# Kernel optimization log

Hardware: AMD Instinct MI355X
Metric: run time of the kernel (lower is better)

Reference implementation:

```python
import jax, jax.numpy as jnp
import numpy as np
from jax import lax

WIN = (9, 9, 9)
EPS = 1e-05


def _sum1d(x, axis, win):
    """Sliding-window sum of size `win` along `axis`, zero-padded (SAME)."""
    pad = win // 2
    pads = [(pad, pad) if a == axis else (0, 0) for a in range(x.ndim)]
    xp = jnp.pad(x, pads)
    c = jnp.cumsum(xp, axis=axis)
    c = jnp.pad(c, [(1, 0) if a == axis else (0, 0) for a in range(x.ndim)])
    n = x.shape[axis]
    return (lax.slice_in_dim(c, win, win + n, axis=axis)
            - lax.slice_in_dim(c, 0, n, axis=axis))


def _box_sum(x):
    """Separable 3D box-filter sum == conv3d with ones([9,9,9]), SAME pad."""
    for axis, w in zip((2, 3, 4), WIN):
        x = _sum1d(x, axis, w)
    return x


def setup_inputs() -> dict:
    key = jax.random.key(0)
    k1, k2 = jax.random.split(key)
    shape = (2, 1, 128, 128, 128)
    y_pred = jax.random.normal(k1, shape, dtype=jnp.float32)
    y_true = jax.random.normal(k2, shape, dtype=jnp.float32)
    return {"y_pred": y_pred, "y_true": y_true}


def reference(y_pred, y_true):
    I = y_true.astype(jnp.float32)
    J = y_pred.astype(jnp.float32)
    win_size = float(np.prod(WIN))  # 729

    I_sum = _box_sum(I)
    J_sum = _box_sum(J)
    I2_sum = _box_sum(I * I)
    J2_sum = _box_sum(J * J)
    IJ_sum = _box_sum(I * J)

    u_I = I_sum / win_size
    u_J = J_sum / win_size

    cross = IJ_sum - u_J * I_sum - u_I * J_sum + u_I * u_J * win_size
    I_var = I2_sum - 2 * u_I * I_sum + u_I * u_I * win_size
    J_var = J2_sum - 2 * u_J * J_sum + u_J * u_J * win_size

    cc_map = cross * cross / (I_var * J_var + EPS)
    return jnp.mean(-cc_map)
```

## Files before the change

kernel.cpp:

```cpp
#include <hip/hip_runtime.h>

#define DSZ 128
#define TX 16
#define TY 16
#define PY 24
#define NVOX 4194304.0f

__global__ void ncc_zero(float* out) { out[0] = 0.0f; }

__global__ __launch_bounds__(256) void ncc_main(const float* __restrict__ Iin,
                                                const float* __restrict__ Jin,
                                                float* __restrict__ out)
{
    const int tx0 = blockIdx.x * TX;
    const int ty0 = blockIdx.y * TY;
    const int b   = blockIdx.z >> 3;
    const int tz0 = (blockIdx.z & 7) * 16;
    const int tid = threadIdx.x;
    const int lx  = tid & 15;
    const int ly  = tid >> 4;

    const float* __restrict__ Ib = Iin + b * (DSZ * DSZ * DSZ);
    const float* __restrict__ Jb = Jin + b * (DSZ * DSZ * DSZ);

    __shared__ float4 s4m[4][PY][17];
    __shared__ float4 s1v[4][PY][5];

    float rb0[9], rb1[9], rb2[9], rb3[9], rb4[9];
#pragma unroll
    for (int i = 0; i < 9; ++i) { rb0[i]=0.f; rb1[i]=0.f; rb2[i]=0.f; rb3[i]=0.f; rb4[i]=0.f; }
    float zs0=0.f, zs1=0.f, zs2=0.f, zs3=0.f, zs4=0.f;
    float acc = 0.f;

    for (int rnd = 0; rnd < 12; ++rnd) {
        if (tid < 192) {
            const int p   = (tid >= 96);
            const int t2  = tid - p * 96;
            const int r   = t2 >> 2;
            const int xg  = t2 & 3;
            const int zp  = tz0 + 2 * rnd + p - 4;
            const int gy  = ty0 + r - 4;
            const int gxb = tx0 + 4 * xg - 4;
            const bool rowok = ((unsigned)zp < (unsigned)DSZ) &&
                               ((unsigned)gy < (unsigned)DSZ);
            const int zoff = (zp * DSZ + gy) * DSZ;

            float vi[12], vj[12];
#pragma unroll
            for (int g = 0; g < 3; ++g) {
                const int gx = gxb + 4 * g;
                float4 va = make_float4(0.f, 0.f, 0.f, 0.f);
                float4 vb = va;
                if (rowok && (unsigned)gx < (unsigned)DSZ) {
                    va = *(const float4*)(Ib + zoff + gx);
                    vb = *(const float4*)(Jb + zoff + gx);
                }
                vi[4*g+0]=va.x; vi[4*g+1]=va.y; vi[4*g+2]=va.z; vi[4*g+3]=va.w;
                vj[4*g+0]=vb.x; vj[4*g+1]=vb.y; vj[4*g+2]=vb.z; vj[4*g+3]=vb.w;
            }

            float wI=0.f, wJ=0.f, wII=0.f, wJJ=0.f, wIJ=0.f;
#pragma unroll
            for (int k = 3; k < 9; ++k) {
                wI += vi[k]; wJ += vj[k];
                wII = fmaf(vi[k], vi[k], wII);
                wJJ = fmaf(vj[k], vj[k], wJJ);
                wIJ = fmaf(vi[k], vj[k], wIJ);
            }
#pragma unroll
            for (int k = 0; k < 3; ++k) {
                wI += vi[k]; wJ += vj[k];
                wII = fmaf(vi[k], vi[k], wII);
                wJJ = fmaf(vj[k], vj[k], wJJ);
                wIJ = fmaf(vi[k], vj[k], wIJ);
            }
            const int sl = (rnd & 1) * 2 + p;
            float mIJ[4];
            s4m[sl][r][4*xg] = make_float4(wI, wJ, wII, wJJ);
            mIJ[0] = wIJ;
#pragma unroll
            for (int j = 1; j < 4; ++j) {
                const float ai = vi[8+j], aj = vj[8+j];
                const float di = vi[j-1], dj = vj[j-1];
                wI += ai - di; wJ += aj - dj;
                wII += fmaf(ai, ai, -di * di);
                wJJ += fmaf(aj, aj, -dj * dj);
                wIJ += fmaf(ai, aj, -di * dj);
                s4m[sl][r][4*xg + j] = make_float4(wI, wJ, wII, wJJ);
                mIJ[j] = wIJ;
            }
            s1v[sl][r][xg] = make_float4(mIJ[0], mIJ[1], mIJ[2], mIJ[3]);
        }
        __syncthreads();

#pragma unroll
        for (int p = 0; p < 2; ++p) {
            const int sl = (rnd & 1) * 2 + p;
            float y0=0.f, y1=0.f, y2=0.f, y3=0.f, y4=0.f;
#pragma unroll
            for (int dy = 0; dy < 9; ++dy) {
                const float4 t = s4m[sl][ly + dy][lx];
                y0 += t.x; y1 += t.y; y2 += t.z; y3 += t.w;
                y4 += ((const float*)&s1v[sl][ly + dy][0])[lx];
            }

            zs0 += y0 - rb0[0]; zs1 += y1 - rb1[0]; zs2 += y2 - rb2[0];
            zs3 += y3 - rb3[0]; zs4 += y4 - rb4[0];
#pragma unroll
            for (int i = 0; i < 8; ++i) {
                rb0[i]=rb0[i+1]; rb1[i]=rb1[i+1]; rb2[i]=rb2[i+1];
                rb3[i]=rb3[i+1]; rb4[i]=rb4[i+1];
            }
            rb0[8]=y0; rb1[8]=y1; rb2[8]=y2; rb3[8]=y3; rb4[8]=y4;

            const int zi = 2 * rnd + p;
            if (zi >= 8) {
                const float inv = 1.0f / 729.0f;
                const float uI = zs0 * inv;
                const float uJ = zs1 * inv;
                const float cross = zs4 - uJ * zs0 - uI * zs1 + uI * uJ * 729.0f;
                const float Ivar  = zs2 - 2.0f * uI * zs0 + uI * uI * 729.0f;
                const float Jvar  = zs3 - 2.0f * uJ * zs1 + uJ * uJ * 729.0f;
                acc += cross * cross / (Ivar * Jvar + 1e-5f);
            }
        }
    }

#pragma unroll
    for (int off = 32; off > 0; off >>= 1) acc += __shfl_down(acc, off);
    __shared__ float wpart[4];
    if ((tid & 63) == 0) wpart[tid >> 6] = acc;
    __syncthreads();
    if (tid == 0) {
        const float s = wpart[0] + wpart[1] + wpart[2] + wpart[3];
        atomicAdd(out, s * (-1.0f / NVOX));
    }
}

extern "C" void kernel_launch(void* const* d_in, const int* in_sizes, int n_in,
                              void* d_out, int out_size, void* d_ws, size_t ws_size,
                              hipStream_t stream)
{
    const float* J = (const float*)d_in[0];
    const float* I = (const float*)d_in[1];
    float* out = (float*)d_out;

    ncc_zero<<<dim3(1), dim3(1), 0, stream>>>(out);
    dim3 grid(DSZ / TX, DSZ / TY, 2 * (DSZ / 16));
    ncc_main<<<grid, dim3(256), 0, stream>>>(I, J, out);
}
```

Baseline: 49.80 us.

## Compute two y-rows per thread with sliding y-sum and ring-buffer z accumulation

The y-direction sum now runs on 128 threads, each producing two adjacent output rows. The second row is derived from the first by a sliding add/subtract, which cuts shared-memory reads. The z-direction running sums use an 8-entry ring buffer indexed by a compile-time slot instead of shifting 9-entry arrays, with the round loop split into 3x4 so the indices stay static. Launch bounds request 3 blocks per CU. The trade-off is that half the threads sit idle during the y/z phase and register pressure goes up.

After: 69.13 us. 38.8% more time.

```diff
diff --git a/kernel.cpp b/kernel.cpp
--- a/kernel.cpp
+++ b/kernel.cpp
@@ -8,17 +8,22 @@
 
 __global__ void ncc_zero(float* out) { out[0] = 0.0f; }
 
-__global__ __launch_bounds__(256) void ncc_main(const float* __restrict__ Iin,
-                                                const float* __restrict__ Jin,
-                                                float* __restrict__ out)
+__device__ __forceinline__ float4 f4add(const float4 a, const float4 b) {
+    return make_float4(a.x + b.x, a.y + b.y, a.z + b.z, a.w + b.w);
+}
+__device__ __forceinline__ float4 f4sub(const float4 a, const float4 b) {
+    return make_float4(a.x - b.x, a.y - b.y, a.z - b.z, a.w - b.w);
+}
+
+__global__ __launch_bounds__(256, 3) void ncc_main(const float* __restrict__ Iin,
+                                                   const float* __restrict__ Jin,
+                                                   float* __restrict__ out)
 {
     const int tx0 = blockIdx.x * TX;
     const int ty0 = blockIdx.y * TY;
     const int b   = blockIdx.z >> 3;
     const int tz0 = (blockIdx.z & 7) * 16;
     const int tid = threadIdx.x;
-    const int lx  = tid & 15;
-    const int ly  = tid >> 4;
 
     const float* __restrict__ Ib = Iin + b * (DSZ * DSZ * DSZ);
     const float* __restrict__ Jb = Jin + b * (DSZ * DSZ * DSZ);
@@ -26,102 +31,117 @@
     __shared__ float4 s4m[4][PY][17];
     __shared__ float4 s1v[4][PY][5];
 
-    float rb0[9], rb1[9], rb2[9], rb3[9], rb4[9];
+    const int lxB = tid & 15;
+    const int ysB = (tid >> 4) & 7;
+
+    float4 rAv[8], rBv[8];
+    float  rAs[8], rBs[8];
+    float4 zA4 = make_float4(0.f, 0.f, 0.f, 0.f), zB4 = zA4;
+    float  zA1 = 0.f, zB1 = 0.f;
 #pragma unroll
-    for (int i = 0; i < 9; ++i) { rb0[i]=0.f; rb1[i]=0.f; rb2[i]=0.f; rb3[i]=0.f; rb4[i]=0.f; }
-    float zs0=0.f, zs1=0.f, zs2=0.f, zs3=0.f, zs4=0.f;
+    for (int i = 0; i < 8; ++i) {
+        rAv[i] = make_float4(0.f, 0.f, 0.f, 0.f);
+        rBv[i] = rAv[i];
+        rAs[i] = 0.f; rBs[i] = 0.f;
+    }
     float acc = 0.f;
 
-    for (int rnd = 0; rnd < 12; ++rnd) {
-        if (tid < 192) {
-            const int p   = (tid >= 96);
-            const int t2  = tid - p * 96;
-            const int r   = t2 >> 2;
-            const int xg  = t2 & 3;
-            const int zp  = tz0 + 2 * rnd + p - 4;
-            const int gy  = ty0 + r - 4;
-            const int gxb = tx0 + 4 * xg - 4;
-            const bool rowok = ((unsigned)zp < (unsigned)DSZ) &&
-                               ((unsigned)gy < (unsigned)DSZ);
-            const int zoff = (zp * DSZ + gy) * DSZ;
+    auto emit_cc = [&](const float4& z4, const float z1) {
+        const float inv = 1.0f / 729.0f;
+        const float uI = z4.x * inv;
+        const float uJ = z4.y * inv;
+        const float cross = z1 - uJ * z4.x - uI * z4.y + uI * uJ * 729.0f;
+        const float Ivar  = z4.z - 2.0f * uI * z4.x + uI * uI * 729.0f;
+        const float Jvar  = z4.w - 2.0f * uJ * z4.y + uJ * uJ * 729.0f;
+        acc += cross * cross / (Ivar * Jvar + 1e-5f);
+    };
 
-            float vi[12], vj[12];
+    for (int mr = 0; mr < 3; ++mr) {
 #pragma unroll
-            for (int g = 0; g < 3; ++g) {
-                const int gx = gxb + 4 * g;
-                float4 va = make_float4(0.f, 0.f, 0.f, 0.f);
-                float4 vb = va;
-                if (rowok && (unsigned)gx < (unsigned)DSZ) {
-                    va = *(const float4*)(Ib + zoff + gx);
-                    vb = *(const float4*)(Jb + zoff + gx);
+        for (int r4 = 0; r4 < 4; ++r4) {
+            if (tid < 192) {
+                const int p   = (tid >= 96);
+                const int t2  = tid - p * 96;
+                const int r   = t2 >> 2;
+                const int xg  = t2 & 3;
+                const int zp  = tz0 + 8 * mr + 2 * r4 + p - 4;
+                const int gy  = ty0 + r - 4;
+                const int gxb = tx0 + 4 * xg - 4;
+                const bool rowok = ((unsigned)zp < (unsigned)DSZ) &&
+                                   ((unsigned)gy < (unsigned)DSZ);
+                const int zoff = (zp * DSZ + gy) * DSZ;
+
+                float vi[12], vj[12];
+#pragma unroll
+                for (int g = 0; g < 3; ++g) {
+                    const int gx = gxb + 4 * g;
+                    float4 va = make_float4(0.f, 0.f, 0.f, 0.f);
+                    float4 vb = va;
+                    if (rowok && (unsigned)gx < (unsigned)DSZ) {
+                        va = *(const float4*)(Ib + zoff + gx);
+                        vb = *(const float4*)(Jb + zoff + gx);
+                    }
+                    vi[4*g+0]=va.x; vi[4*g+1]=va.y; vi[4*g+2]=va.z; vi[4*g+3]=va.w;
+                    vj[4*g+0]=vb.x; vj[4*g+1]=vb.y; vj[4*g+2]=vb.z; vj[4*g+3]=vb.w;
                 }
-                vi[4*g+0]=va.x; vi[4*g+1]=va.y; vi[4*g+2]=va.z; vi[4*g+3]=va.w;
-                vj[4*g+0]=vb.x; vj[4*g+1]=vb.y; vj[4*g+2]=vb.z; vj[4*g+3]=vb.w;
+
+                float wI=0.f, wJ=0.f, wII=0.f, wJJ=0.f, wIJ=0.f;
+#pragma unroll
+                for (int k = 0; k < 9; ++k) {
+                    wI += vi[k]; wJ += vj[k];
+                    wII = fmaf(vi[k], vi[k], wII);
+                    wJJ = fmaf(vj[k], vj[k], wJJ);
+                    wIJ = fmaf(vi[k], vj[k], wIJ);
+                }
+                const int sl = (r4 & 1) * 2 + p;
+                float mIJ[4];
+                s4m[sl][r][4*xg] = make_float4(wI, wJ, wII, wJJ);
+                mIJ[0] = wIJ;
+#pragma unroll
+                for (int j = 1; j < 4; ++j) {
+                    const float ai = vi[8+j], aj = vj[8+j];
+                    const float di = vi[j-1], dj = vj[j-1];
+                    wI += ai - di; wJ += aj - dj;
+                    wII += fmaf(ai, ai, -di * di);
+                    wJJ += fmaf(aj, aj, -dj * dj);
+                    wIJ += fmaf(ai, aj, -di * dj);
+                    s4m[sl][r][4*xg + j] = make_float4(wI, wJ, wII, wJJ);
+                    mIJ[j] = wIJ;
+                }
+                s1v[sl][r][xg] = make_float4(mIJ[0], mIJ[1], mIJ[2], mIJ[3]);
             }
+            __syncthreads();
 
-            float wI=0.f, wJ=0.f, wII=0.f, wJJ=0.f, wIJ=0.f;
+            if (tid >= 128) {
 #pragma unroll
-            for (int k = 3; k < 9; ++k) {
-                wI += vi[k]; wJ += vj[k];
-                wII = fmaf(vi[k], vi[k], wII);
-                wJJ = fmaf(vj[k], vj[k], wJJ);
-                wIJ = fmaf(vi[k], vj[k], wIJ);
-            }
+                for (int p = 0; p < 2; ++p) {
+                    const int sl = (r4 & 1) * 2 + p;
+                    const int k  = (2 * r4 + p) & 7;
+
+                    const float4 row0v = s4m[sl][2*ysB + 0][lxB];
+                    const float  row0s = ((const float*)&s1v[sl][2*ysB + 0][0])[lxB];
+                    float4 c4 = row0v;
+                    float  c1 = row0s;
 #pragma unroll
-            for (int k = 0; k < 3; ++k) {
-                wI += vi[k]; wJ += vj[k];
-                wII = fmaf(vi[k], vi[k], wII);
-                wJJ = fmaf(vj[k], vj[k], wJJ);
-                wIJ = fmaf(vi[k], vj[k], wIJ);
-            }
-            const int sl = (rnd & 1) * 2 + p;
-            float mIJ[4];
-            s4m[sl][r][4*xg] = make_float4(wI, wJ, wII, wJJ);
-            mIJ[0] = wIJ;
-#pragma unroll
-            for (int j = 1; j < 4; ++j) {
-                const float ai = vi[8+j], aj = vj[8+j];
-                const float di = vi[j-1], dj = vj[j-1];
-                wI += ai - di; wJ += aj - dj;
-                wII += fmaf(ai, ai, -di * di);
-                wJJ += fmaf(aj, aj, -dj * dj);
-                wIJ += fmaf(ai, aj, -di * dj);
-                s4m[sl][r][4*xg + j] = make_float4(wI, wJ, wII, wJJ);
-                mIJ[j] = wIJ;
-            }
-            s1v[sl][r][xg] = make_float4(mIJ[0], mIJ[1], mIJ[2], mIJ[3]);
-        }
-        __syncthreads();
+                    for (int dy = 1; dy < 9; ++dy) {
+                        c4 = f4add(c4, s4m[sl][2*ysB + dy][lxB]);
+                        c1 += ((const float*)&s1v[sl][2*ysB + dy][0])[lxB];
+                    }
+                    const float4 r9v = s4m[sl][2*ysB + 9][lxB];
+                    const float  r9s = ((const float*)&s1v[sl][2*ysB + 9][0])[lxB];
+                    const float4 d4 = f4add(f4sub(c4, row0v), r9v);
+                    const float  d1 = c1 - row0s + r9s;
 
-#pragma unroll
-        for (int p = 0; p < 2; ++p) {
-            const int sl = (rnd & 1) * 2 + p;
-            float y0=0.f, y1=0.f, y2=0.f, y3=0.f, y4=0.f;
-#pragma unroll
-            for (int dy = 0; dy < 9; ++dy) {
-                const float4 t = s4m[sl][ly + dy][lx];
-                y0 += t.x; y1 += t.y; y2 += t.z; y3 += t.w;
-                y4 += ((const float*)&s1v[sl][ly + dy][0])[lx];
-            }
+                    zA4 = f4add(zA4, c4); zA1 += c1;
+                    if (mr > 0) emit_cc(zA4, zA1);
+                    zA4 = f4sub(zA4, rAv[k]); zA1 -= rAs[k];
+                    rAv[k] = c4; rAs[k] = c1;
 
-            zs0 += y0 - rb0[0]; zs1 += y1 - rb1[0]; zs2 += y2 - rb2[0];
-            zs3 += y3 - rb3[0]; zs4 += y4 - rb4[0];
-#pragma unroll
-            for (int i = 0; i < 8; ++i) {
-                rb0[i]=rb0[i+1]; rb1[i]=rb1[i+1]; rb2[i]=rb2[i+1];
-                rb3[i]=rb3[i+1]; rb4[i]=rb4[i+1];
-            }
-            rb0[8]=y0; rb1[8]=y1; rb2[8]=y2; rb3[8]=y3; rb4[8]=y4;
-
-            const int zi = 2 * rnd + p;
-            if (zi >= 8) {
-                const float inv = 1.0f / 729.0f;
-                const float uI = zs0 * inv;
-                const float uJ = zs1 * inv;
-                const float cross = zs4 - uJ * zs0 - uI * zs1 + uI * uJ * 729.0f;
-                const float Ivar  = zs2 - 2.0f * uI * zs0 + uI * uI * 729.0f;
-                const float Jvar  = zs3 - 2.0f * uJ * zs1 + uJ * uJ * 729.0f;
-                acc += cross * cross / (Ivar * Jvar + 1e-5f);
+                    zB4 = f4add(zB4, d4); zB1 += d1;
+                    if (mr > 0) emit_cc(zB4, zB1);
+                    zB4 = f4sub(zB4, rBv[k]); zB1 -= rBs[k];
+                    rBv[k] = d4; rBs[k] = d1;
+                }
             }
         }
     }
```
